# Kernel tuning notes

Hardware: AMD Instinct MI355X
Metric: run time of the kernel (lower is better)

Reference implementation:

```python
import jax, jax.numpy as jnp
import numpy as np
from jax import lax

# Model constants (from init_kwargs)
N_B, N_T, N_IN, N_REC, N_OUT = 64, 1000, 80, 512, 20
DT, TAU_M, TAU_O = 1.0, 20.0, 20.0
ALPHA = float(np.exp(-DT / TAU_M))   # membrane leak
KAPPA = float(np.exp(-DT / TAU_O))   # output leak
THR = 1.0
B_O = 0.0
GAIN = (0.5, 0.1, 0.5)


def setup_inputs() -> dict:
    key = jax.random.key(0)
    k = jax.random.split(key, 5)
    x = jax.random.normal(k[0], (N_B, N_T, N_IN), jnp.float32)
    # kaiming_normal_ (fan_in mode, std = sqrt(2/fan_in)) scaled by gain
    w_in = jax.random.normal(k[1], (N_REC, N_IN), jnp.float32) * (np.sqrt(2.0 / N_IN) * GAIN[0])
    w_rec = jax.random.normal(k[2], (N_REC, N_REC), jnp.float32) * (np.sqrt(2.0 / N_REC) * GAIN[1])
    w_out = jax.random.normal(k[3], (N_OUT, N_REC), jnp.float32) * (np.sqrt(2.0 / N_REC) * GAIN[2])
    # per-step torch.randn noise, materialized deterministically
    noise = jax.random.normal(k[4], (N_T, N_B, N_REC), jnp.float32)
    # full-length sequences: pack/pad roundtrip becomes identity
    seq_lengths = jnp.full((N_B,), N_T, dtype=jnp.int32)
    return {"x": x, "w_in": w_in, "w_rec": w_rec, "w_out": w_out,
            "noise": noise, "seq_lengths": seq_lengths}


def reference(x, w_in, w_rec, w_out, noise, seq_lengths):
    """LIF spiking RNN forward (inference path, do_training=False).

    x:     (B, T, n_in)
    noise: (T, B, n_rec)  -- the per-step torch.randn injected into v
    Returns (softmax_vo (B,T,n_out), vo (T,B,n_out)) as in the torch module.
    """
    n_b, n_t, _ = x.shape
    n_rec = w_rec.shape[0]
    n_out = w_out.shape[0]
    dtype = x.dtype

    # zero the recurrent self-connections (w_rec *= 1 - eye)
    w_rec_m = w_rec * (1.0 - jnp.eye(n_rec, dtype=w_rec.dtype))

    # padded inputs are zero beyond seq_lengths; here all lengths == n_t so
    # the pack/pad roundtrip is identity. mask anyway for faithfulness.
    t_idx = jnp.arange(n_t)[None, :, None]                     # (1,T,1)
    x_padded = jnp.where(t_idx < seq_lengths[:, None, None], x, 0.0)

    def step(carry, inp):
        v, z, vo = carry
        x_t, noise_t1 = inp
        # v[t+1] = alpha*v[t] + z[t]@w_rec.T + x[t]@w_in.T - z[t]*thr + noise
        v_new = (ALPHA * v
                 + z @ w_rec_m.T
                 + x_t @ w_in.T
                 - z * THR
                 + noise_t1)
        z_new = (v_new > THR).astype(dtype)          # hard threshold spike
        vo_new = KAPPA * vo + z_new @ w_out.T + B_O  # leaky readout
        return (v_new, z_new, vo_new), vo_new

    init = (jnp.zeros((n_b, n_rec), dtype),
            jnp.zeros((n_b, n_rec), dtype),
            jnp.zeros((n_b, n_out), dtype))
    # loop t = 0 .. n_t-2 consumes x[:, t] and noise[t+1]
    xs = (jnp.swapaxes(x_padded, 0, 1)[:-1], noise[1:])
    _, vo_seq = lax.scan(step, init, xs)             # (T-1, B, n_out)

    vo = jnp.concatenate([jnp.zeros((1, n_b, n_out), dtype), vo_seq], axis=0)  # (T,B,O)
    softmax_vo = jax.nn.softmax(jnp.transpose(vo, (1, 0, 2)), axis=2)          # (B,T,O)
    return softmax_vo, vo
```

## Files before the change

kernel.cpp:

```cpp
#include <hip/hip_runtime.h>

#define N_B   64
#define N_T   1000
#define N_IN  80
#define N_REC 512
#define N_OUT 20
#define THR 1.0f

constexpr float ALPHA = 0.9512294245007140f;
constexpr float KAPPA = 0.9512294245007140f;

__global__ void k_transpose(const float* __restrict__ w_rec, float* __restrict__ wT) {
    int i = blockIdx.x * blockDim.x + threadIdx.x;
    if (i >= 513 * N_REC) return;
    int j = i >> 9;
    int r = i & 511;
    float v = 0.0f;
    if (j < N_REC && r != j) v = w_rec[r * N_REC + j];
    wT[i] = v;
}

__global__ __launch_bounds__(512, 2) void k_inj(
    const float* __restrict__ x, const float* __restrict__ w_in,
    const float* __restrict__ noise, const int* __restrict__ seq,
    float* __restrict__ inj, int t0, int t1)
{
    const int r = threadIdx.x;
    float wreg[N_IN];
#pragma unroll
    for (int i = 0; i < N_IN; ++i) wreg[i] = w_in[r * N_IN + i];

    const int P = (t1 - t0) * N_B;
    for (int p = blockIdx.x; p < P; p += gridDim.x) {
        int pt = p >> 6;
        int b  = p & 63;
        int t  = t0 + pt;
        float acc = noise[((size_t)t * N_B + b) * N_REC + r];
        if (t - 1 < seq[b]) {
            const float* xr = x + ((size_t)b * N_T + (t - 1)) * N_IN;
#pragma unroll
            for (int i = 0; i < N_IN; ++i) acc = fmaf(wreg[i], xr[i], acc);
        }
        inj[(size_t)p * N_REC + r] = acc;
    }
}

__global__ __launch_bounds__(512, 1) void k_scan(
    const float* __restrict__ wT, const float* __restrict__ inj,
    const float* __restrict__ w_out, float* __restrict__ out_vo,
    int t0, int t1,
    float* __restrict__ st_v, unsigned long long* __restrict__ st_zm,
    float* __restrict__ st_vo)
{
    const int b    = blockIdx.x;
    const int tid  = threadIdx.x;
    const int w    = tid >> 6;
    const int lane = tid & 63;
    const int g    = tid >> 7;
    const int c    = tid & 127;
    const unsigned long long lt = (1ull << lane) - 1ull;
    const int DUMMY = N_REC << 11;

    __shared__ int lists[N_REC];
    __shared__ unsigned long long zm[8];
    __shared__ int pc[8];
    __shared__ float4 tmp_part[4][128];
    __shared__ float tmp[N_OUT][16];
    __shared__ alignas(16) float zf[N_REC];

    float wvo[32];
    {
        int o = tid >> 4, s = tid & 15;
        if (tid < 320) {
#pragma unroll
            for (int i = 0; i < 32; ++i)
                wvo[i] = w_out[(size_t)o * N_REC + s * 32 + i];
        } else {
#pragma unroll
            for (int i = 0; i < 32; ++i) wvo[i] = 0.0f;
        }
    }

    float v;
    int z;
    float vo = 0.0f;
    int npad = 0;

    if (t0 == 1) {
        v = 0.0f; z = 0;
    } else {
        v = st_v[(size_t)b * N_REC + tid];
        unsigned long long m = st_zm[b * 8 + w];
        z = (int)((m >> lane) & 1ull);
        if (tid < 8) zm[tid] = st_zm[b * 8 + tid];
        if (tid < N_OUT) vo = st_vo[b * N_OUT + tid];
        __syncthreads();
        unsigned long long bm0 = zm[w];
        if (lane == 0) pc[w] = __popcll(bm0);
        __syncthreads();
        int basep = 0, ntot = 0;
#pragma unroll
        for (int ww = 0; ww < 8; ++ww) {
            int s_ = pc[ww];
            if (ww < w) basep += s_;
            ntot += s_;
        }
        if (z) lists[basep + __popcll(bm0 & lt)] = tid << 11;
        npad = (ntot + 31) & ~31;
        { int i = ntot + tid; if (i < npad) lists[i] = DUMMY; }
        __syncthreads();
    }

    float injn = __builtin_nontemporal_load(inj + ((size_t)0 * N_B + b) * N_REC + tid);

    for (int t = t0; t < t1; ++t) {
        float injv = injn;

        if (t > t0 && tid < N_OUT) {
            float s = 0.0f;
#pragma unroll
            for (int cc = 0; cc < 16; ++cc) s += tmp[tid][cc];
            vo = KAPPA * vo + s;
            out_vo[((size_t)(t - 1) * N_B + b) * N_OUT + tid] = vo;
        }

        float4 acc; acc.x = 0.0f; acc.y = 0.0f; acc.z = 0.0f; acc.w = 0.0f;
        {
            const int q = npad >> 2;
            if (q > 0) {
                const int* lc = lists + g * q;
                const int nb = q >> 3;
                int jv = lc[lane & 7];
                float4 vA[8];
#pragma unroll
                for (int u = 0; u < 8; ++u) {
                    int off = __builtin_amdgcn_readlane(jv, u);
                    vA[u] = *(const float4*)((const char*)wT + off + (c << 4));
                }
                for (int k = 1; k < nb; ++k) {
                    int jv2 = lc[(k << 3) + (lane & 7)];
                    float4 vB[8];
#pragma unroll
                    for (int u = 0; u < 8; ++u) {
                        int off = __builtin_amdgcn_readlane(jv2, u);
                        vB[u] = *(const float4*)((const char*)wT + off + (c << 4));
                    }
#pragma unroll
                    for (int u = 0; u < 8; ++u) {
                        acc.x += vA[u].x; acc.y += vA[u].y;
                        acc.z += vA[u].z; acc.w += vA[u].w;
                        vA[u] = vB[u];
                    }
                }
#pragma unroll
                for (int u = 0; u < 8; ++u) {
                    acc.x += vA[u].x; acc.y += vA[u].y;
                    acc.z += vA[u].z; acc.w += vA[u].w;
                }
            }
        }
        tmp_part[g][c] = acc;

        if (t + 1 < t1)
            injn = __builtin_nontemporal_load(
                inj + ((size_t)(t + 1 - t0) * N_B + b) * N_REC + tid);

        __syncthreads();

        {
            const float* tp = (const float*)tmp_part;
            float accn = tp[tid] + tp[512 + tid] + tp[1024 + tid] + tp[1536 + tid];
            v = ALPHA * v + accn + injv - (z ? THR : 0.0f);
            z = v > THR;
            zf[tid] = z ? 1.0f : 0.0f;
        }
        unsigned long long bm = __ballot(z);
        if (lane == 0) { zm[w] = bm; pc[w] = __popcll(bm); }

        __syncthreads();

        {
            int basep = 0, ntot = 0;
#pragma unroll
            for (int ww = 0; ww < 8; ++ww) {
                int s_ = pc[ww];
                if (ww < w) basep += s_;
                ntot += s_;
            }
            if (z) lists[basep + __popcll(bm & lt)] = tid << 11;
            int npn = (ntot + 31) & ~31;
            { int i = ntot + tid; if (i < npn) lists[i] = DUMMY; }
            npad = npn;
        }
        if (tid < 320) {
            int o = tid >> 4, s = tid & 15;
            const float4* zp = ((const float4*)zf) + (s << 3);
            float sa = 0.0f;
#pragma unroll
            for (int i = 0; i < 8; ++i) {
                float4 zv = zp[i];
                sa = fmaf(wvo[4 * i + 0], zv.x, sa);
                sa = fmaf(wvo[4 * i + 1], zv.y, sa);
                sa = fmaf(wvo[4 * i + 2], zv.z, sa);
                sa = fmaf(wvo[4 * i + 3], zv.w, sa);
            }
            tmp[o][s] = sa;
        }

        __syncthreads();
    }

    if (tid < N_OUT) {
        float s = 0.0f;
#pragma unroll
        for (int cc = 0; cc < 16; ++cc) s += tmp[tid][cc];
        vo = KAPPA * vo + s;
        out_vo[((size_t)(t1 - 1) * N_B + b) * N_OUT + tid] = vo;
    }

    st_v[(size_t)b * N_REC + tid] = v;
    if (lane == 0) st_zm[b * 8 + w] = zm[w];
    if (tid < N_OUT) st_vo[b * N_OUT + tid] = vo;
}

__global__ void k_softmax(const float* __restrict__ vo_seq,
                          float* __restrict__ out_sm,
                          float* __restrict__ out_vo0)
{
    int idx = blockIdx.x * blockDim.x + threadIdx.x;
    if (idx >= N_B * N_T) return;
    int b = idx / N_T;
    int t = idx - b * N_T;
    float vals[N_OUT];
    if (t == 0) {
#pragma unroll
        for (int o = 0; o < N_OUT; ++o) {
            vals[o] = 0.0f;
            out_vo0[(size_t)b * N_OUT + o] = 0.0f;
        }
    } else {
#pragma unroll
        for (int o = 0; o < N_OUT; ++o)
            vals[o] = vo_seq[((size_t)t * N_B + b) * N_OUT + o];
    }
    float mx = vals[0];
#pragma unroll
    for (int o = 1; o < N_OUT; ++o) mx = fmaxf(mx, vals[o]);
    float s = 0.0f;
#pragma unroll
    for (int o = 0; o < N_OUT; ++o) { vals[o] = expf(vals[o] - mx); s += vals[o]; }
    float inv = 1.0f / s;
#pragma unroll
    for (int o = 0; o < N_OUT; ++o)
        out_sm[((size_t)b * N_T + t) * N_OUT + o] = vals[o] * inv;
}

extern "C" void kernel_launch(void* const* d_in, const int* in_sizes, int n_in,
                              void* d_out, int out_size, void* d_ws, size_t ws_size,
                              hipStream_t stream)
{
    (void)in_sizes; (void)n_in; (void)out_size;
    const float* x     = (const float*)d_in[0];
    const float* w_in  = (const float*)d_in[1];
    const float* w_rec = (const float*)d_in[2];
    const float* w_out = (const float*)d_in[3];
    const float* noise = (const float*)d_in[4];
    const int*   seq   = (const int*)d_in[5];

    float* out    = (float*)d_out;
    float* out_sm = out;
    float* out_vo = out + (size_t)N_B * N_T * N_OUT;

    char* ws = (char*)d_ws;
    float* wT = (float*)ws;
    size_t off = (size_t)513 * N_REC * sizeof(float);
    float* st_v = (float*)(ws + off);                off += (size_t)N_B * N_REC * sizeof(float);
    unsigned long long* st_zm = (unsigned long long*)(ws + off); off += (size_t)N_B * 8 * sizeof(unsigned long long);
    float* st_vo = (float*)(ws + off);               off += (size_t)N_B * N_OUT * sizeof(float);
    off = (off + 255) & ~(size_t)255;
    float* inj = (float*)(ws + off);

    size_t avail = (ws_size > off) ? (ws_size - off) : 0;
    size_t step_bytes = (size_t)N_B * N_REC * sizeof(float);
    long max_steps = (long)(avail / step_bytes);
    int tchunk = (int)((max_steps > (N_T - 1)) ? (N_T - 1) : max_steps);
    if (tchunk < 1) tchunk = 1;

    k_transpose<<<dim3((513 * N_REC + 255) / 256), dim3(256), 0, stream>>>(w_rec, wT);

    for (int t0 = 1; t0 < N_T; t0 += tchunk) {
        int t1 = t0 + tchunk; if (t1 > N_T) t1 = N_T;
        k_inj<<<dim3(512), dim3(512), 0, stream>>>(x, w_in, noise, seq, inj, t0, t1);
        k_scan<<<dim3(N_B), dim3(512), 0, stream>>>(wT, inj, w_out, out_vo,
                                                    t0, t1, st_v, st_zm, st_vo);
    }

    k_softmax<<<dim3((N_B * N_T + 255) / 256), dim3(256), 0, stream>>>(out_vo, out_sm, out_vo);
}
```

Before: 2.811 ms.

## Defer readout matvec to next step, drop a barrier, preload spike lists

Moves the w_out readout matvec and vo accumulation off the end of each timestep: the matvec now runs in the next step after the recurrent gather, and the reduction runs before the second barrier. This removes one __syncthreads per timestep from the serial scan. It also pads the spike buffer and transposes the partial-sum layout to avoid LDS bank conflicts, loads the whole spike list into registers once via readlane, and prefetches noise in the injection kernel. The result depends on the zfp buffer not being overwritten before it is consumed, and this ordering is subtle.

New measurement: 2.615 ms. 7.0% less time.

```diff
diff --git a/kernel.cpp b/kernel.cpp
--- a/kernel.cpp
+++ b/kernel.cpp
@@ -31,11 +31,21 @@
     for (int i = 0; i < N_IN; ++i) wreg[i] = w_in[r * N_IN + i];
 
     const int P = (t1 - t0) * N_B;
-    for (int p = blockIdx.x; p < P; p += gridDim.x) {
+    const int stride = gridDim.x;
+
+    auto nz = [&](int p) -> float {
+        int pt = p >> 6, b = p & 63, t = t0 + pt;
+        return __builtin_nontemporal_load(noise + ((size_t)t * N_B + b) * N_REC + r);
+    };
+
+    int p = blockIdx.x;
+    float nxt = (p < P) ? nz(p) : 0.0f;
+    for (; p < P; p += stride) {
+        float acc = nxt;
+        if (p + stride < P) nxt = nz(p + stride);
         int pt = p >> 6;
         int b  = p & 63;
         int t  = t0 + pt;
-        float acc = noise[((size_t)t * N_B + b) * N_REC + r];
         if (t - 1 < seq[b]) {
             const float* xr = x + ((size_t)b * N_T + (t - 1)) * N_IN;
 #pragma unroll
@@ -65,8 +75,8 @@
     __shared__ unsigned long long zm[8];
     __shared__ int pc[8];
     __shared__ float4 tmp_part[4][128];
-    __shared__ float tmp[N_OUT][16];
-    __shared__ alignas(16) float zf[N_REC];
+    __shared__ float tmp2[16][21];
+    __shared__ alignas(16) float zfp[16 * 36];
 
     float wvo[32];
     {
@@ -116,34 +126,29 @@
     for (int t = t0; t < t1; ++t) {
         float injv = injn;
 
-        if (t > t0 && tid < N_OUT) {
-            float s = 0.0f;
-#pragma unroll
-            for (int cc = 0; cc < 16; ++cc) s += tmp[tid][cc];
-            vo = KAPPA * vo + s;
-            out_vo[((size_t)(t - 1) * N_B + b) * N_OUT + tid] = vo;
-        }
-
         float4 acc; acc.x = 0.0f; acc.y = 0.0f; acc.z = 0.0f; acc.w = 0.0f;
         {
             const int q = npad >> 2;
             if (q > 0) {
-                const int* lc = lists + g * q;
+                int jv  = lists[g * q + lane];
+                int jv2 = (q > 64) ? lists[g * q + 64 + (lane & 63)] : 0;
+                const char* wb = (const char*)wT + (c << 4);
                 const int nb = q >> 3;
-                int jv = lc[lane & 7];
                 float4 vA[8];
 #pragma unroll
                 for (int u = 0; u < 8; ++u) {
                     int off = __builtin_amdgcn_readlane(jv, u);
-                    vA[u] = *(const float4*)((const char*)wT + off + (c << 4));
+                    vA[u] = *(const float4*)(wb + off);
                 }
                 for (int k = 1; k < nb; ++k) {
-                    int jv2 = lc[(k << 3) + (lane & 7)];
                     float4 vB[8];
 #pragma unroll
                     for (int u = 0; u < 8; ++u) {
-                        int off = __builtin_amdgcn_readlane(jv2, u);
-                        vB[u] = *(const float4*)((const char*)wT + off + (c << 4));
+                        int ug = (k << 3) + u;
+                        int off = (ug < 64)
+                            ? __builtin_amdgcn_readlane(jv,  ug)
+                            : __builtin_amdgcn_readlane(jv2, ug - 64);
+                        vB[u] = *(const float4*)(wb + off);
                     }
 #pragma unroll
                     for (int u = 0; u < 8; ++u) {
@@ -159,6 +164,20 @@
                 }
             }
         }
+        if (t > t0 && tid < 320) {
+            int o = tid >> 4, s = tid & 15;
+            const float4* zp = (const float4*)(zfp + s * 36);
+            float sa = 0.0f;
+#pragma unroll
+            for (int i = 0; i < 8; ++i) {
+                float4 zv = zp[i];
+                sa = fmaf(wvo[4 * i + 0], zv.x, sa);
+                sa = fmaf(wvo[4 * i + 1], zv.y, sa);
+                sa = fmaf(wvo[4 * i + 2], zv.z, sa);
+                sa = fmaf(wvo[4 * i + 3], zv.w, sa);
+            }
+            tmp2[s][o] = sa;
+        }
         tmp_part[g][c] = acc;
 
         if (t + 1 < t1)
@@ -172,11 +191,17 @@
             float accn = tp[tid] + tp[512 + tid] + tp[1024 + tid] + tp[1536 + tid];
             v = ALPHA * v + accn + injv - (z ? THR : 0.0f);
             z = v > THR;
-            zf[tid] = z ? 1.0f : 0.0f;
+            zfp[(tid >> 5) * 36 + (tid & 31)] = z ? 1.0f : 0.0f;
         }
         unsigned long long bm = __ballot(z);
         if (lane == 0) { zm[w] = bm; pc[w] = __popcll(bm); }
-
+        if (t > t0 && tid < N_OUT) {
+            float s = 0.0f;
+#pragma unroll
+            for (int ss = 0; ss < 16; ++ss) s += tmp2[ss][tid];
+            vo = KAPPA * vo + s;
+            out_vo[((size_t)(t - 1) * N_B + b) * N_OUT + tid] = vo;
+        }
         __syncthreads();
 
         {
@@ -192,35 +217,35 @@
             { int i = ntot + tid; if (i < npn) lists[i] = DUMMY; }
             npad = npn;
         }
-        if (tid < 320) {
-            int o = tid >> 4, s = tid & 15;
-            const float4* zp = ((const float4*)zf) + (s << 3);
-            float sa = 0.0f;
-#pragma unroll
-            for (int i = 0; i < 8; ++i) {
-                float4 zv = zp[i];
-                sa = fmaf(wvo[4 * i + 0], zv.x, sa);
-                sa = fmaf(wvo[4 * i + 1], zv.y, sa);
-                sa = fmaf(wvo[4 * i + 2], zv.z, sa);
-                sa = fmaf(wvo[4 * i + 3], zv.w, sa);
-            }
-            tmp[o][s] = sa;
-        }
-
-        __syncthreads();
-    }
-
+        __syncthreads();
+    }
+
+    if (tid < 320) {
+        int o = tid >> 4, s = tid & 15;
+        const float4* zp = (const float4*)(zfp + s * 36);
+        float sa = 0.0f;
+#pragma unroll
+        for (int i = 0; i < 8; ++i) {
+            float4 zv = zp[i];
+            sa = fmaf(wvo[4 * i + 0], zv.x, sa);
+            sa = fmaf(wvo[4 * i + 1], zv.y, sa);
+            sa = fmaf(wvo[4 * i + 2], zv.z, sa);
+            sa = fmaf(wvo[4 * i + 3], zv.w, sa);
+        }
+        tmp2[s][o] = sa;
+    }
+    __syncthreads();
     if (tid < N_OUT) {
         float s = 0.0f;
 #pragma unroll
-        for (int cc = 0; cc < 16; ++cc) s += tmp[tid][cc];
+        for (int ss = 0; ss < 16; ++ss) s += tmp2[ss][tid];
         vo = KAPPA * vo + s;
         out_vo[((size_t)(t1 - 1) * N_B + b) * N_OUT + tid] = vo;
+        st_vo[b * N_OUT + tid] = vo;
     }
 
     st_v[(size_t)b * N_REC + tid] = v;
     if (lane == 0) st_zm[b * 8 + w] = zm[w];
-    if (tid < N_OUT) st_vo[b * N_OUT + tid] = vo;
 }
 
 __global__ void k_softmax(const float* __restrict__ vo_seq,
```
